# Performance work log

Hardware: AMD Instinct MI355X
Metric: run time of the kernel (lower is better)

The kernel has to match this reference:

```python
import jax, jax.numpy as jnp
import numpy as np

NEG_SLOPE = 0.01  # torch.nn.LeakyReLU default


def setup_inputs() -> dict:
    key = jax.random.key(0)
    ks = jax.random.split(key, 9)
    B, S, F1, F2, N, M, E, L = 2, 256, 512, 512, 20000, 2, 320000, 3
    x = jax.random.normal(ks[0], (B, S, F1), dtype=jnp.float32)
    nodes = jax.random.normal(ks[1], (N, M, F2), dtype=jnp.float32)
    edge_index = jax.random.randint(ks[2], (2, E), 0, N, dtype=jnp.int32)
    Wp = jax.random.normal(ks[3], (F1, F2), dtype=jnp.float32) * 0.02  # torch Linear weight [out,in]
    bp = jax.random.normal(ks[4], (F1,), dtype=jnp.float32) * 0.02
    gcn_W = jax.random.normal(ks[5], (L, S, S), dtype=jnp.float32) * 0.05  # stored as [in,out]
    gcn_b = jax.random.normal(ks[6], (L, S), dtype=jnp.float32) * 0.02
    w_bp = jax.random.normal(ks[7], (S,), dtype=jnp.float32) * 0.05
    b_bp = jax.random.normal(ks[8], (1,), dtype=jnp.float32) * 0.02
    return {"x": x, "nodes": nodes, "edge_index": edge_index, "Wp": Wp, "bp": bp,
            "gcn_W": gcn_W, "gcn_b": gcn_b, "w_bp": w_bp, "b_bp": b_bp}


def reference(x, nodes, edge_index, Wp, bp, gcn_W, gcn_b, w_bp, b_bp):
    # Eval mode: dropout layers are identity.
    N = nodes.shape[0]
    L = gcn_W.shape[0]
    proj = nodes @ Wp.T + bp                         # [N, M, F1]
    score = jnp.einsum('bsk,nmk->bsn', x, proj)      # sum over M and F1 -> [B, S, N]
    h = score.transpose(0, 2, 1)                     # beliefs [B, N, S]

    # GCN normalization with self-loops: D^{-1/2} (A + I) D^{-1/2}
    src, dst = edge_index[0], edge_index[1]
    loop = jnp.arange(N, dtype=edge_index.dtype)
    row = jnp.concatenate([src, loop])               # message sources
    col = jnp.concatenate([dst, loop])               # message targets
    deg = jnp.zeros((N,), dtype=h.dtype).at[col].add(1.0)
    dinv = deg ** -0.5                               # deg >= 1 due to self-loops
    norm = dinv[row] * dinv[col]                     # [E+N]

    for l in range(L):
        hw = h @ gcn_W[l]                            # [B, N, S]
        msg = hw[:, row, :] * norm[None, :, None]    # gather + scale
        agg = jnp.zeros_like(hw).at[:, col, :].add(msg) + gcn_b[l]
        h = jax.nn.leaky_relu(agg, NEG_SLOPE)

    # belief_projection: Linear(S, 1) then squeeze -> [B, N]
    return h @ w_bp + b_bp[0]
```

## Files before the change

kernel.cpp:

```cpp
#include <hip/hip_runtime.h>
#include <cstddef>
#include <cstdint>

#define NN 20000

typedef short frag16 __attribute__((ext_vector_type(8)));
typedef float f32x4 __attribute__((ext_vector_type(4)));

__device__ inline unsigned short f32_to_bf16(float f) {
    uint32_t u = __float_as_uint(f);
    u += 0x7FFFu + ((u >> 16) & 1u);
    return (unsigned short)(u >> 16);
}

__device__ inline void dec8_add(uint4 v, float* a) {
    a[0] += __uint_as_float(v.x << 16);
    a[1] += __uint_as_float(v.x & 0xffff0000u);
    a[2] += __uint_as_float(v.y << 16);
    a[3] += __uint_as_float(v.y & 0xffff0000u);
    a[4] += __uint_as_float(v.z << 16);
    a[5] += __uint_as_float(v.z & 0xffff0000u);
    a[6] += __uint_as_float(v.w << 16);
    a[7] += __uint_as_float(v.w & 0xffff0000u);
}

__global__ __launch_bounds__(256) void prep(
    const float* __restrict__ nodes, const float* __restrict__ x,
    const float* __restrict__ gcn_W, const float* __restrict__ bp,
    const int* __restrict__ src, const int* __restrict__ dst,
    unsigned short* __restrict__ nsum16, unsigned short* __restrict__ WT,
    float* __restrict__ Tf, float* __restrict__ cvec,
    int* __restrict__ cnt, int* __restrict__ csr, int E)
{
    __shared__ __align__(16) char shmem[8704];
    const int blk = blockIdx.x, tid = threadIdx.x;

    if (blk < 64) {
        float* As = (float*)shmem;
        float* Bs = As + 1024;
        int t = blk;
        int b = t >> 5, rem = t & 31;
        int s0 = (rem >> 3) * 64, f0 = (rem & 7) * 64;
        const float* W1 = gcn_W;
        const float* xb = x + (size_t)b * 256 * 512;
        int kk = tid >> 4, c4 = (tid & 15) << 2;
        int tm = tid >> 4, tn = tid & 15;
        float acc[4][4] = {};
        float4 av = *(const float4*)(W1 + (size_t)kk * 256 + s0 + c4);
        float4 bv = *(const float4*)(xb + (size_t)kk * 512 + f0 + c4);
        for (int k0 = 0; k0 < 256; k0 += 16) {
            __syncthreads();
            *(float4*)&As[kk * 64 + c4] = av;
            *(float4*)&Bs[kk * 64 + c4] = bv;
            __syncthreads();
            if (k0 + 16 < 256) {
                av = *(const float4*)(W1 + (size_t)(k0 + 16 + kk) * 256 + s0 + c4);
                bv = *(const float4*)(xb + (size_t)(k0 + 16 + kk) * 512 + f0 + c4);
            }
            #pragma unroll
            for (int k = 0; k < 16; ++k) {
                float a[4], bb[4];
                *(float4*)a  = *(const float4*)&As[k * 64 + (tm << 2)];
                *(float4*)bb = *(const float4*)&Bs[k * 64 + (tn << 2)];
                #pragma unroll
                for (int i = 0; i < 4; ++i)
                    #pragma unroll
                    for (int j = 0; j < 4; ++j) acc[i][j] += a[i] * bb[j];
            }
        }
        #pragma unroll
        for (int i = 0; i < 4; ++i) {
            int row = b * 256 + s0 + (tm << 2) + i;
            *(float4*)(Tf + (size_t)row * 512 + f0 + (tn << 2)) =
                make_float4(acc[i][0], acc[i][1], acc[i][2], acc[i][3]);
        }
    } else if (blk < 96) {
        unsigned short (*tsh)[68] = (unsigned short(*)[68])shmem;
        int t = blk - 64;
        int l = t >> 4, rem = t & 15;
        int c0 = (rem & 3) * 64, r0 = (rem >> 2) * 64;
        const float* inp = gcn_W + (size_t)(l + 1) * 65536;
        unsigned short* outp = WT + (size_t)l * 65536;
        int tx = tid & 15, ty = tid >> 4;
        #pragma unroll
        for (int rr = 0; rr < 4; ++rr) {
            int r = ty * 4 + rr;
            float4 v = *(const float4*)(inp + (size_t)(r0 + r) * 256 + c0 + tx * 4);
            tsh[tx * 4 + 0][r] = f32_to_bf16(v.x);
            tsh[tx * 4 + 1][r] = f32_to_bf16(v.y);
            tsh[tx * 4 + 2][r] = f32_to_bf16(v.z);
            tsh[tx * 4 + 3][r] = f32_to_bf16(v.w);
        }
        __syncthreads();
        #pragma unroll
        for (int cc = 0; cc < 4; ++cc) {
            int c = ty * 4 + cc;
            ushort4 o = *(ushort4*)&tsh[c][tx * 4];
            *(ushort4*)(outp + (size_t)(c0 + c) * 256 + r0 + tx * 4) = o;
        }
    } else if (blk < 224) {
        int row = (blk - 96) * 4 + (tid >> 6);
        int lane = tid & 63;
        const float* xr = x + (size_t)row * 512;
        float s = 0.f;
        #pragma unroll
        for (int k = 0; k < 512; k += 64) s += xr[k + lane] * bp[k + lane];
        #pragma unroll
        for (int off = 32; off; off >>= 1) s += __shfl_down(s, off);
        if (lane == 0) cvec[row] = 2.0f * s;
    } else if (blk < 224 + 2512) {
        int g = (blk - 224) * 256 + tid;
        int n = g >> 5, c = (g & 31) << 4;
        uint4 o0, o1;
        if (n < NN) {
            const float* r0 = nodes + (size_t)n * 1024 + c;
            const float* r1 = r0 + 512;
            float4 a0 = *(const float4*)(r0 + 0),  a1 = *(const float4*)(r0 + 4);
            float4 a2 = *(const float4*)(r0 + 8),  a3 = *(const float4*)(r0 + 12);
            float4 b0 = *(const float4*)(r1 + 0),  b1 = *(const float4*)(r1 + 4);
            float4 b2 = *(const float4*)(r1 + 8),  b3 = *(const float4*)(r1 + 12);
            o0.x = ((uint32_t)f32_to_bf16(a0.y + b0.y) << 16) | f32_to_bf16(a0.x + b0.x);
            o0.y = ((uint32_t)f32_to_bf16(a0.w + b0.w) << 16) | f32_to_bf16(a0.z + b0.z);
            o0.z = ((uint32_t)f32_to_bf16(a1.y + b1.y) << 16) | f32_to_bf16(a1.x + b1.x);
            o0.w = ((uint32_t)f32_to_bf16(a1.w + b1.w) << 16) | f32_to_bf16(a1.z + b1.z);
            o1.x = ((uint32_t)f32_to_bf16(a2.y + b2.y) << 16) | f32_to_bf16(a2.x + b2.x);
            o1.y = ((uint32_t)f32_to_bf16(a2.w + b2.w) << 16) | f32_to_bf16(a2.z + b2.z);
            o1.z = ((uint32_t)f32_to_bf16(a3.y + b3.y) << 16) | f32_to_bf16(a3.x + b3.x);
            o1.w = ((uint32_t)f32_to_bf16(a3.w + b3.w) << 16) | f32_to_bf16(a3.z + b3.z);
        } else {
            o0 = make_uint4(0, 0, 0, 0); o1 = o0;
        }
        *(uint4*)(nsum16 + (size_t)n * 512 + c) = o0;
        *(uint4*)(nsum16 + (size_t)n * 512 + c + 8) = o1;
    } else {
        int e = (blk - 2736) * 256 + tid;
        if (e < E) {
            int d = dst[e];
            int pos = atomicAdd(&cnt[d], 1);
            if (pos < 64) csr[(d << 6) + pos] = src[e];
        }
    }
}

__global__ __launch_bounds__(256) void mid(
    const float* __restrict__ Tf, const float* __restrict__ Wp,
    const float* __restrict__ gcn_W, const float* __restrict__ cvec,
    unsigned short* __restrict__ Ub, float* __restrict__ cb2)
{
    const int blk = blockIdx.x, tid = threadIdx.x;
    if (blk >= 64) {
        int idx = (blk - 64) * 256 + tid;
        int b = idx >> 8, s = idx & 255;
        float sum = 0.f;
        for (int sp = 0; sp < 256; ++sp)
            sum += gcn_W[(size_t)sp * 256 + s] * cvec[b * 256 + sp];
        cb2[idx] = sum;
        return;
    }
    __shared__ float As[16][68];
    __shared__ float Bs[16][64];
    int bm = (blk >> 3) * 64, bn = (blk & 7) * 64;
    int arow = tid >> 2, acol = (tid & 3) << 2;
    int brow = tid >> 4, bcol = (tid & 15) << 2;
    int tm = tid >> 4, tn = tid & 15;
    float acc[4][4] = {};
    float4 av = *(const float4*)(Tf + (size_t)(bm + arow) * 512 + acol);
    float4 bv = *(const float4*)(Wp + (size_t)brow * 512 + bn + bcol);
    for (int k0 = 0; k0 < 512; k0 += 16) {
        __syncthreads();
        As[acol + 0][arow] = av.x; As[acol + 1][arow] = av.y;
        As[acol + 2][arow] = av.z; As[acol + 3][arow] = av.w;
        *(float4*)&Bs[brow][bcol] = bv;
        __syncthreads();
        if (k0 + 16 < 512) {
            av = *(const float4*)(Tf + (size_t)(bm + arow) * 512 + k0 + 16 + acol);
            bv = *(const float4*)(Wp + (size_t)(k0 + 16 + brow) * 512 + bn + bcol);
        }
        #pragma unroll
        for (int k = 0; k < 16; ++k) {
            float a[4], b[4];
            *(float4*)a = *(const float4*)&As[k][tm << 2];
            *(float4*)b = *(const float4*)&Bs[k][tn << 2];
            #pragma unroll
            for (int i = 0; i < 4; ++i)
                #pragma unroll
                for (int j = 0; j < 4; ++j) acc[i][j] += a[i] * b[j];
        }
    }
    #pragma unroll
    for (int i = 0; i < 4; ++i) {
        int row = bm + (tm << 2) + i;
        ushort4 o;
        o.x = f32_to_bf16(acc[i][0]); o.y = f32_to_bf16(acc[i][1]);
        o.z = f32_to_bf16(acc[i][2]); o.w = f32_to_bf16(acc[i][3]);
        *(ushort4*)(Ub + (size_t)row * 512 + bn + (tn << 2)) = o;
    }
}

__global__ __launch_bounds__(256) void mgemm(
    const unsigned short* __restrict__ A, const unsigned short* __restrict__ BT,
    int K, int N, int mode,
    const float* __restrict__ cb2, const int* __restrict__ cnt,
    unsigned short* __restrict__ C)
{
    __shared__ __align__(16) unsigned short As[128 * 32];
    __shared__ __align__(16) unsigned short Bs[128 * 32];
    const int bm = blockIdx.y * 128, bn = blockIdx.x * 128;
    const int tid = threadIdx.x;
    const int lane = tid & 63, w = tid >> 6;
    const int wm = (w >> 1) << 6, wn = (w & 1) << 6;
    const int r = lane & 15, q = lane >> 4;

    f32x4 acc[4][4] = {};

    for (int k0 = 0; k0 < K; k0 += 32) {
        __syncthreads();
        #pragma unroll
        for (int t = 0; t < 2; ++t) {
            int c = t * 256 + w * 64 + lane;
            int row = c >> 2, col = (c & 3) << 3;
            __builtin_amdgcn_global_load_lds(
                (const __attribute__((address_space(1))) void*)(A + (size_t)(bm + row) * K + k0 + col),
                (__attribute__((address_space(3))) void*)(As + (size_t)(t * 256 + w * 64) * 8),
                16, 0, 0);
            __builtin_amdgcn_global_load_lds(
                (const __attribute__((address_space(1))) void*)(BT + (size_t)(bn + row) * K + k0 + col),
                (__attribute__((address_space(3))) void*)(Bs + (size_t)(t * 256 + w * 64) * 8),
                16, 0, 0);
        }
        __syncthreads();
        frag16 af[4], bf[4];
        #pragma unroll
        for (int i = 0; i < 4; ++i)
            af[i] = *(const frag16*)(As + ((wm + i * 16 + r) << 5) + (q << 3));
        #pragma unroll
        for (int j = 0; j < 4; ++j)
            bf[j] = *(const frag16*)(Bs + ((wn + j * 16 + r) << 5) + (q << 3));
        #pragma unroll
        for (int i = 0; i < 4; ++i)
            #pragma unroll
            for (int j = 0; j < 4; ++j)
                acc[i][j] = __builtin_amdgcn_mfma_f32_16x16x32_bf16(af[i], bf[j], acc[i][j], 0, 0, 0);
    }

    #pragma unroll
    for (int i = 0; i < 4; ++i) {
        #pragma unroll
        for (int rg = 0; rg < 4; ++rg) {
            int m = bm + wm + i * 16 + (q << 2) + rg;
            float sc;
            int b2 = 0, node = m;
            if (mode == 1) {
                int nc = m > NN - 1 ? NN - 1 : m;
                sc = rsqrtf((float)cnt[nc] + 1.0f);
            } else {
                b2 = m >= NN;
                node = m - b2 * NN;
                int nc = node > NN - 1 ? NN - 1 : node;
                sc = rsqrtf((float)cnt[nc] + 1.0f);
                if (node > 20095) node = 20095;
            }
            #pragma unroll
            for (int j = 0; j < 4; ++j) {
                int n = bn + wn + j * 16 + r;
                if (mode == 1) {
                    float v = (acc[i][j][rg] + cb2[n]) * sc;
                    C[(size_t)m * 512 + n] = f32_to_bf16(v);
                } else {
                    float v = acc[i][j][rg] * sc;
                    C[(size_t)node * 512 + (b2 << 8) + n] = f32_to_bf16(v);
                }
            }
        }
    }
}

__global__ __launch_bounds__(256) void aggregate_x(
    const unsigned short* __restrict__ hw, const int* __restrict__ cnt,
    const int* __restrict__ csr, const float* __restrict__ bias,
    unsigned short* __restrict__ hout,
    const float* __restrict__ w_bp, float* __restrict__ pout)
{
    __shared__ int sidx[2048];
    __shared__ int sdeg[32];
    const int s  = blockIdx.x & 7;
    const int nb = blockIdx.x >> 3;
    const int tid = threadIdx.x;
    const int g = tid >> 3;
    const int j = tid & 7;
    const int n = nb * 32 + g;

    {
        const int4* cp = (const int4*)(csr + ((size_t)nb << 11));
        int4 v0 = cp[tid * 2];
        int4 v1 = cp[tid * 2 + 1];
        *(int4*)&sidx[tid * 8]     = v0;
        *(int4*)&sidx[tid * 8 + 4] = v1;
        if (tid < 32) {
            int d = cnt[nb * 32 + tid];
            sdeg[tid] = d > 64 ? 64 : d;
        }
    }
    __syncthreads();

    const unsigned short* rowp = hw + (s << 6) + (j << 3);
    const int deg = sdeg[g];
    const int* gi = sidx + (g << 6);

    float acc[8] = {};
    dec8_add(*(const uint4*)(rowp + (size_t)n * 512), acc);

    int e = 0;
    for (; e + 8 <= deg; e += 8) {
        int s0 = gi[e + 0], s1 = gi[e + 1], s2 = gi[e + 2], s3 = gi[e + 3];
        int s4 = gi[e + 4], s5 = gi[e + 5], s6 = gi[e + 6], s7 = gi[e + 7];
        uint4 u0 = *(const uint4*)(rowp + (size_t)s0 * 512);
        uint4 u1 = *(const uint4*)(rowp + (size_t)s1 * 512);
        uint4 u2 = *(const uint4*)(rowp + (size_t)s2 * 512);
        uint4 u3 = *(const uint4*)(rowp + (size_t)s3 * 512);
        uint4 u4 = *(const uint4*)(rowp + (size_t)s4 * 512);
        uint4 u5 = *(const uint4*)(rowp + (size_t)s5 * 512);
        uint4 u6 = *(const uint4*)(rowp + (size_t)s6 * 512);
        uint4 u7 = *(const uint4*)(rowp + (size_t)s7 * 512);
        dec8_add(u0, acc); dec8_add(u1, acc); dec8_add(u2, acc); dec8_add(u3, acc);
        dec8_add(u4, acc); dec8_add(u5, acc); dec8_add(u6, acc); dec8_add(u7, acc);
    }
    for (; e < deg; ++e) {
        dec8_add(*(const uint4*)(rowp + (size_t)gi[e] * 512), acc);
    }

    float dn = rsqrtf((float)deg + 1.0f);
    int colb = ((s & 3) << 6) + (j << 3);
    float bl[8];
    *(float4*)&bl[0] = *(const float4*)(bias + colb);
    *(float4*)&bl[4] = *(const float4*)(bias + colb + 4);
    float v[8];
    #pragma unroll
    for (int t = 0; t < 8; ++t) {
        v[t] = fmaf(dn, acc[t], bl[t]);
        v[t] = v[t] > 0.f ? v[t] : 0.01f * v[t];
    }

    if (hout) {
        int b = s >> 2;
        uint4 o;
        o.x = ((uint32_t)f32_to_bf16(v[1]) << 16) | f32_to_bf16(v[0]);
        o.y = ((uint32_t)f32_to_bf16(v[3]) << 16) | f32_to_bf16(v[2]);
        o.z = ((uint32_t)f32_to_bf16(v[5]) << 16) | f32_to_bf16(v[4]);
        o.w = ((uint32_t)f32_to_bf16(v[7]) << 16) | f32_to_bf16(v[6]);
        *(uint4*)(hout + ((size_t)(b * NN + n)) * 256 + colb) = o;
    } else {
        float w4[8];
        *(float4*)&w4[0] = *(const float4*)(w_bp + colb);
        *(float4*)&w4[4] = *(const float4*)(w_bp + colb + 4);
        float sum = 0.f;
        #pragma unroll
        for (int t = 0; t < 8; ++t) sum += v[t] * w4[t];
        sum += __shfl_xor(sum, 1);
        sum += __shfl_xor(sum, 2);
        sum += __shfl_xor(sum, 4);
        if (j == 0) pout[s * NN + n] = sum;
    }
}

__global__ __launch_bounds__(256) void finishk(
    const float* __restrict__ pout, const float* __restrict__ b_bp,
    float* __restrict__ out)
{
    int i = blockIdx.x * 256 + threadIdx.x;
    if (i < 2 * NN) {
        int b = i >= NN;
        int n = i - b * NN;
        const float* p = pout + b * 4 * NN + n;
        out[i] = b_bp[0] + p[0] + p[NN] + p[2 * NN] + p[3 * NN];
    }
}

extern "C" void kernel_launch(void* const* d_in, const int* in_sizes, int n_in,
                              void* d_out, int out_size, void* d_ws, size_t ws_size,
                              hipStream_t stream) {
    const float* x     = (const float*)d_in[0];
    const float* nodes = (const float*)d_in[1];
    const int*   eidx  = (const int*)d_in[2];
    const float* Wp    = (const float*)d_in[3];
    const float* bp    = (const float*)d_in[4];
    const float* gcn_W = (const float*)d_in[5];
    const float* gcn_b = (const float*)d_in[6];
    const float* w_bp  = (const float*)d_in[7];
    const float* b_bp  = (const float*)d_in[8];
    const int E = in_sizes[2] / 2;

    char* w = (char*)d_ws;
    auto alloc = [&](size_t bytes) { char* p = w; w += (bytes + 255) & ~(size_t)255; return p; };
    unsigned short* nsum16 = (unsigned short*)alloc((size_t)20096 * 512 * 2);
    unsigned short* hw16   = (unsigned short*)alloc((size_t)20096 * 512 * 2);
    unsigned short* hA     = (unsigned short*)alloc((size_t)40192 * 256 * 2);
    unsigned short* hB     = (unsigned short*)alloc((size_t)40192 * 256 * 2);
    float* Tf  = (float*)alloc((size_t)512 * 512 * 4);
    unsigned short* Ub = (unsigned short*)alloc((size_t)512 * 512 * 2);
    unsigned short* WT = (unsigned short*)alloc((size_t)2 * 256 * 256 * 2);
    float* cvec = (float*)alloc(512 * 4);
    float* cb2  = (float*)alloc(512 * 4);
    float* pout = (float*)alloc((size_t)8 * NN * 4);
    int*   cnt  = (int*)alloc((size_t)NN * 4);
    int*   csr  = (int*)alloc((size_t)NN * 64 * 4);

    hipMemsetAsync(cnt, 0, (size_t)NN * 4, stream);

    const int cntBlks = (E + 255) / 256;
    prep<<<cntBlks + 64 + 2512 + 32 + 128, 256, 0, stream>>>(
        nodes, x, gcn_W, bp, eidx, eidx + E, nsum16, WT, Tf, cvec, cnt, csr, E);
    mid<<<66, 256, 0, stream>>>(Tf, Wp, gcn_W, cvec, Ub, cb2);

    mgemm<<<dim3(4, 157), 256, 0, stream>>>(nsum16, Ub, 512, 512, 1, cb2, cnt, hw16);

    aggregate_x<<<5000, 256, 0, stream>>>(hw16, cnt, csr, gcn_b + 0, hA, w_bp, pout);
    mgemm<<<dim3(2, 313), 256, 0, stream>>>(hA, WT, 256, 256, 2, nullptr, cnt, hw16);
    aggregate_x<<<5000, 256, 0, stream>>>(hw16, cnt, csr, gcn_b + 256, hB, w_bp, pout);
    mgemm<<<dim3(2, 313), 256, 0, stream>>>(hB, WT + 65536, 256, 256, 2, nullptr, cnt, hw16);
    aggregate_x<<<5000, 256, 0, stream>>>(hw16, cnt, csr, gcn_b + 512, nullptr, w_bp, pout);
    finishk<<<157, 256, 0, stream>>>(pout, b_bp, (float*)d_out);
}
```

Before: 339.8 us.

## Partition CSR build by destination range and deepen gather unroll in aggregation

The edge-to-CSR build moves to the front of the fused prep launch. Each edge chunk is now handled by 8 blocks, and each block only processes destinations in its own 2500-node range, so atomics and csr writes from one block stay in a narrower address region. This costs 8x redundant reads of dst. Separately, the aggregation gather loop issues 16 independent row loads per iteration instead of 8, raising memory-level parallelism at the cost of more registers.

```diff
diff --git a/kernel.cpp b/kernel.cpp
--- a/kernel.cpp
+++ b/kernel.cpp
@@ -34,11 +34,27 @@
 {
     __shared__ __align__(16) char shmem[8704];
     const int blk = blockIdx.x, tid = threadIdx.x;
-
-    if (blk < 64) {
+    const int csrB = ((E + 2047) >> 11) << 3;
+
+    if (blk < csrB) {
+        const int part = blk & 7;
+        const int ebase = (blk >> 3) << 11;
+        const int d0 = part * 2500, d1 = d0 + 2500;
+        #pragma unroll
+        for (int k = 0; k < 8; ++k) {
+            int e = ebase + k * 256 + tid;
+            if (e < E) {
+                int d = dst[e];
+                if (d >= d0 && d < d1) {
+                    int pos = atomicAdd(&cnt[d], 1);
+                    if (pos < 64) csr[(d << 6) + pos] = src[e];
+                }
+            }
+        }
+    } else if (blk < csrB + 64) {
         float* As = (float*)shmem;
         float* Bs = As + 1024;
-        int t = blk;
+        int t = blk - csrB;
         int b = t >> 5, rem = t & 31;
         int s0 = (rem >> 3) * 64, f0 = (rem & 7) * 64;
         const float* W1 = gcn_W;
@@ -74,9 +90,9 @@
             *(float4*)(Tf + (size_t)row * 512 + f0 + (tn << 2)) =
                 make_float4(acc[i][0], acc[i][1], acc[i][2], acc[i][3]);
         }
-    } else if (blk < 96) {
+    } else if (blk < csrB + 96) {
         unsigned short (*tsh)[68] = (unsigned short(*)[68])shmem;
-        int t = blk - 64;
+        int t = blk - csrB - 64;
         int l = t >> 4, rem = t & 15;
         int c0 = (rem & 3) * 64, r0 = (rem >> 2) * 64;
         const float* inp = gcn_W + (size_t)(l + 1) * 65536;
@@ -98,8 +114,8 @@
             ushort4 o = *(ushort4*)&tsh[c][tx * 4];
             *(ushort4*)(outp + (size_t)(c0 + c) * 256 + r0 + tx * 4) = o;
         }
-    } else if (blk < 224) {
-        int row = (blk - 96) * 4 + (tid >> 6);
+    } else if (blk < csrB + 224) {
+        int row = (blk - csrB - 96) * 4 + (tid >> 6);
         int lane = tid & 63;
         const float* xr = x + (size_t)row * 512;
         float s = 0.f;
@@ -108,8 +124,8 @@
         #pragma unroll
         for (int off = 32; off; off >>= 1) s += __shfl_down(s, off);
         if (lane == 0) cvec[row] = 2.0f * s;
-    } else if (blk < 224 + 2512) {
-        int g = (blk - 224) * 256 + tid;
+    } else {
+        int g = (blk - csrB - 224) * 256 + tid;
         int n = g >> 5, c = (g & 31) << 4;
         uint4 o0, o1;
         if (n < NN) {
@@ -132,13 +148,6 @@
         }
         *(uint4*)(nsum16 + (size_t)n * 512 + c) = o0;
         *(uint4*)(nsum16 + (size_t)n * 512 + c + 8) = o1;
-    } else {
-        int e = (blk - 2736) * 256 + tid;
-        if (e < E) {
-            int d = dst[e];
-            int pos = atomicAdd(&cnt[d], 1);
-            if (pos < 64) csr[(d << 6) + pos] = src[e];
-        }
     }
 }
 
@@ -311,19 +320,22 @@
     dec8_add(*(const uint4*)(rowp + (size_t)n * 512), acc);
 
     int e = 0;
-    for (; e + 8 <= deg; e += 8) {
-        int s0 = gi[e + 0], s1 = gi[e + 1], s2 = gi[e + 2], s3 = gi[e + 3];
-        int s4 = gi[e + 4], s5 = gi[e + 5], s6 = gi[e + 6], s7 = gi[e + 7];
-        uint4 u0 = *(const uint4*)(rowp + (size_t)s0 * 512);
-        uint4 u1 = *(const uint4*)(rowp + (size_t)s1 * 512);
-        uint4 u2 = *(const uint4*)(rowp + (size_t)s2 * 512);
-        uint4 u3 = *(const uint4*)(rowp + (size_t)s3 * 512);
-        uint4 u4 = *(const uint4*)(rowp + (size_t)s4 * 512);
-        uint4 u5 = *(const uint4*)(rowp + (size_t)s5 * 512);
-        uint4 u6 = *(const uint4*)(rowp + (size_t)s6 * 512);
-        uint4 u7 = *(const uint4*)(rowp + (size_t)s7 * 512);
-        dec8_add(u0, acc); dec8_add(u1, acc); dec8_add(u2, acc); dec8_add(u3, acc);
-        dec8_add(u4, acc); dec8_add(u5, acc); dec8_add(u6, acc); dec8_add(u7, acc);
+    for (; e + 16 <= deg; e += 16) {
+        uint4 u[16];
+        #pragma unroll
+        for (int t = 0; t < 16; ++t)
+            u[t] = *(const uint4*)(rowp + (size_t)gi[e + t] * 512);
+        #pragma unroll
+        for (int t = 0; t < 16; ++t) dec8_add(u[t], acc);
+    }
+    if (e + 8 <= deg) {
+        uint4 u[8];
+        #pragma unroll
+        for (int t = 0; t < 8; ++t)
+            u[t] = *(const uint4*)(rowp + (size_t)gi[e + t] * 512);
+        #pragma unroll
+        for (int t = 0; t < 8; ++t) dec8_add(u[t], acc);
+        e += 8;
     }
     for (; e < deg; ++e) {
         dec8_add(*(const uint4*)(rowp + (size_t)gi[e] * 512), acc);
@@ -407,8 +419,8 @@
 
     hipMemsetAsync(cnt, 0, (size_t)NN * 4, stream);
 
-    const int cntBlks = (E + 255) / 256;
-    prep<<<cntBlks + 64 + 2512 + 32 + 128, 256, 0, stream>>>(
+    const int csrB = ((E + 2047) / 2048) * 8;
+    prep<<<csrB + 224 + 2512, 256, 0, stream>>>(
         nodes, x, gcn_W, bp, eidx, eidx + E, nsum16, WT, Tf, cvec, cnt, csr, E);
     mid<<<66, 256, 0, stream>>>(Tf, Wp, gcn_W, cvec, Ub, cb2);
 
```

Result: slower. 359.7 us (+5.9%).

## Retile mid GEMM into smaller tiles and remap mgemm blocks per XCD

Applied to the files above, without the earlier changes.

The small fp32 GEMM in mid moves from 64 blocks with 64x64 tiles to 256 blocks with 32x32 tiles, so more CUs take part, at the cost of less register reuse and dropping the prefetch of the next k-slice. mgemm now uses a 1D grid and remaps the block id so that consecutive tiles land on the same XCD, which is meant to improve L2 locality for shared A/B rows across MI355X chiplets. The remapping also adds index arithmetic, and the tile mapping depends on the mode-specific column count.

```diff
diff --git a/kernel.cpp b/kernel.cpp
--- a/kernel.cpp
+++ b/kernel.cpp
@@ -148,8 +148,8 @@
     unsigned short* __restrict__ Ub, float* __restrict__ cb2)
 {
     const int blk = blockIdx.x, tid = threadIdx.x;
-    if (blk >= 64) {
-        int idx = (blk - 64) * 256 + tid;
+    if (blk >= 256) {
+        int idx = (blk - 256) * 256 + tid;
         int b = idx >> 8, s = idx & 255;
         float sum = 0.f;
         for (int sp = 0; sp < 256; ++sp)
@@ -157,43 +157,33 @@
         cb2[idx] = sum;
         return;
     }
-    __shared__ float As[16][68];
-    __shared__ float Bs[16][64];
-    int bm = (blk >> 3) * 64, bn = (blk & 7) * 64;
-    int arow = tid >> 2, acol = (tid & 3) << 2;
-    int brow = tid >> 4, bcol = (tid & 15) << 2;
-    int tm = tid >> 4, tn = tid & 15;
-    float acc[4][4] = {};
-    float4 av = *(const float4*)(Tf + (size_t)(bm + arow) * 512 + acol);
-    float4 bv = *(const float4*)(Wp + (size_t)brow * 512 + bn + bcol);
+    __shared__ float As[16][33];
+    __shared__ float Bs[16][34];
+    int bm = (blk >> 4) << 5, bn = (blk & 15) << 5;
+    int ar = tid >> 3, ac = (tid & 7) << 1;
+    int br = tid >> 4, bc = (tid & 15) << 1;
+    int tm = (tid >> 4) << 1, tn = (tid & 15) << 1;
+    float acc[2][2] = {};
     for (int k0 = 0; k0 < 512; k0 += 16) {
+        float2 av = *(const float2*)(Tf + (size_t)(bm + ar) * 512 + k0 + ac);
+        float2 bv = *(const float2*)(Wp + (size_t)(k0 + br) * 512 + bn + bc);
         __syncthreads();
-        As[acol + 0][arow] = av.x; As[acol + 1][arow] = av.y;
-        As[acol + 2][arow] = av.z; As[acol + 3][arow] = av.w;
-        *(float4*)&Bs[brow][bcol] = bv;
+        As[ac][ar] = av.x; As[ac + 1][ar] = av.y;
+        Bs[br][bc] = bv.x; Bs[br][bc + 1] = bv.y;
         __syncthreads();
-        if (k0 + 16 < 512) {
-            av = *(const float4*)(Tf + (size_t)(bm + arow) * 512 + k0 + 16 + acol);
-            bv = *(const float4*)(Wp + (size_t)(k0 + 16 + brow) * 512 + bn + bcol);
-        }
         #pragma unroll
         for (int k = 0; k < 16; ++k) {
-            float a[4], b[4];
-            *(float4*)a = *(const float4*)&As[k][tm << 2];
-            *(float4*)b = *(const float4*)&Bs[k][tn << 2];
-            #pragma unroll
-            for (int i = 0; i < 4; ++i)
-                #pragma unroll
-                for (int j = 0; j < 4; ++j) acc[i][j] += a[i] * b[j];
+            float a0 = As[k][tm], a1 = As[k][tm + 1];
+            float b0 = Bs[k][tn], b1 = Bs[k][tn + 1];
+            acc[0][0] += a0 * b0; acc[0][1] += a0 * b1;
+            acc[1][0] += a1 * b0; acc[1][1] += a1 * b1;
         }
     }
     #pragma unroll
-    for (int i = 0; i < 4; ++i) {
-        int row = bm + (tm << 2) + i;
-        ushort4 o;
+    for (int i = 0; i < 2; ++i) {
+        ushort2 o;
         o.x = f32_to_bf16(acc[i][0]); o.y = f32_to_bf16(acc[i][1]);
-        o.z = f32_to_bf16(acc[i][2]); o.w = f32_to_bf16(acc[i][3]);
-        *(ushort4*)(Ub + (size_t)row * 512 + bn + (tn << 2)) = o;
+        *(ushort2*)(Ub + (size_t)(bm + tm + i) * 512 + bn + tn) = o;
     }
 }
 
@@ -205,11 +195,17 @@
 {
     __shared__ __align__(16) unsigned short As[128 * 32];
     __shared__ __align__(16) unsigned short Bs[128 * 32];
-    const int bm = blockIdx.y * 128, bn = blockIdx.x * 128;
+    const int nwg = gridDim.x;
+    const int orig = blockIdx.x;
+    const int xcd = orig & 7, jj = orig >> 3;
+    const int q = nwg >> 3, r = nwg & 7;
+    const int wgid = (xcd < r ? xcd * (q + 1) : r * (q + 1) + (xcd - r) * q) + jj;
+    const int lx = (mode == 1) ? 2 : 1;
+    const int bm = (wgid >> lx) * 128, bn = (wgid & ((1 << lx) - 1)) * 128;
     const int tid = threadIdx.x;
     const int lane = tid & 63, w = tid >> 6;
     const int wm = (w >> 1) << 6, wn = (w & 1) << 6;
-    const int r = lane & 15, q = lane >> 4;
+    const int r16 = lane & 15, q16 = lane >> 4;
 
     f32x4 acc[4][4] = {};
 
@@ -232,10 +228,10 @@
         frag16 af[4], bf[4];
         #pragma unroll
         for (int i = 0; i < 4; ++i)
-            af[i] = *(const frag16*)(As + ((wm + i * 16 + r) << 5) + (q << 3));
+            af[i] = *(const frag16*)(As + ((wm + i * 16 + r16) << 5) + (q16 << 3));
         #pragma unroll
         for (int j = 0; j < 4; ++j)
-            bf[j] = *(const frag16*)(Bs + ((wn + j * 16 + r) << 5) + (q << 3));
+            bf[j] = *(const frag16*)(Bs + ((wn + j * 16 + r16) << 5) + (q16 << 3));
         #pragma unroll
         for (int i = 0; i < 4; ++i)
             #pragma unroll
@@ -247,7 +243,7 @@
     for (int i = 0; i < 4; ++i) {
         #pragma unroll
         for (int rg = 0; rg < 4; ++rg) {
-            int m = bm + wm + i * 16 + (q << 2) + rg;
+            int m = bm + wm + i * 16 + (q16 << 2) + rg;
             float sc;
             int b2 = 0, node = m;
             if (mode == 1) {
@@ -262,7 +258,7 @@
             }
             #pragma unroll
             for (int j = 0; j < 4; ++j) {
-                int n = bn + wn + j * 16 + r;
+                int n = bn + wn + j * 16 + r16;
                 if (mode == 1) {
                     float v = (acc[i][j][rg] + cb2[n]) * sc;
                     C[(size_t)m * 512 + n] = f32_to_bf16(v);
@@ -410,14 +406,14 @@
     const int cntBlks = (E + 255) / 256;
     prep<<<cntBlks + 64 + 2512 + 32 + 128, 256, 0, stream>>>(
         nodes, x, gcn_W, bp, eidx, eidx + E, nsum16, WT, Tf, cvec, cnt, csr, E);
-    mid<<<66, 256, 0, stream>>>(Tf, Wp, gcn_W, cvec, Ub, cb2);
-
-    mgemm<<<dim3(4, 157), 256, 0, stream>>>(nsum16, Ub, 512, 512, 1, cb2, cnt, hw16);
+    mid<<<258, 256, 0, stream>>>(Tf, Wp, gcn_W, cvec, Ub, cb2);
+
+    mgemm<<<628, 256, 0, stream>>>(nsum16, Ub, 512, 512, 1, cb2, cnt, hw16);
 
     aggregate_x<<<5000, 256, 0, stream>>>(hw16, cnt, csr, gcn_b + 0, hA, w_bp, pout);
-    mgemm<<<dim3(2, 313), 256, 0, stream>>>(hA, WT, 256, 256, 2, nullptr, cnt, hw16);
+    mgemm<<<626, 256, 0, stream>>>(hA, WT, 256, 256, 2, nullptr, cnt, hw16);
     aggregate_x<<<5000, 256, 0, stream>>>(hw16, cnt, csr, gcn_b + 256, hB, w_bp, pout);
-    mgemm<<<dim3(2, 313), 256, 0, stream>>>(hB, WT + 65536, 256, 256, 2, nullptr, cnt, hw16);
+    mgemm<<<626, 256, 0, stream>>>(hB, WT + 65536, 256, 256, 2, nullptr, cnt, hw16);
     aggregate_x<<<5000, 256, 0, stream>>>(hw16, cnt, csr, gcn_b + 512, nullptr, w_bp, pout);
     finishk<<<157, 256, 0, stream>>>(pout, b_bp, (float*)d_out);
 }
```

New measurement: 345.6 us. No clear change (+1.7%).

## Load MFMA fragments directly from global memory and shrink mgemm N-tile

Applied to the files above, without the earlier changes.

Removes the LDS staging and both barriers per k-step from the bf16 MFMA GEMM. Each wave now reads its A and B fragments straight from global memory into registers. The block tile drops from 128x128 to 128x64, and the grid doubles in x to compensate. The goal is to cut synchronization and LDS traffic and to raise the block count, at the cost of relying on L1/L2 for cross-wave reuse and issuing more global loads.

```diff
diff --git a/kernel.cpp b/kernel.cpp
--- a/kernel.cpp
+++ b/kernel.cpp
@@ -203,43 +203,31 @@
     const float* __restrict__ cb2, const int* __restrict__ cnt,
     unsigned short* __restrict__ C)
 {
-    __shared__ __align__(16) unsigned short As[128 * 32];
-    __shared__ __align__(16) unsigned short Bs[128 * 32];
-    const int bm = blockIdx.y * 128, bn = blockIdx.x * 128;
+    const int bm = blockIdx.y * 128, bn = blockIdx.x * 64;
     const int tid = threadIdx.x;
     const int lane = tid & 63, w = tid >> 6;
-    const int wm = (w >> 1) << 6, wn = (w & 1) << 6;
-    const int r = lane & 15, q = lane >> 4;
-
-    f32x4 acc[4][4] = {};
-
+    const int wm = (w >> 1) << 6, wn = (w & 1) << 5;
+    const int r16 = lane & 15, q16 = lane >> 4;
+
+    const unsigned short* Ap = A  + (size_t)(bm + wm + r16) * K + (q16 << 3);
+    const unsigned short* Bp = BT + (size_t)(bn + wn + r16) * K + (q16 << 3);
+    const size_t a16 = (size_t)16 * K;
+
+    f32x4 acc[4][2] = {};
+
+    #pragma unroll 2
     for (int k0 = 0; k0 < K; k0 += 32) {
-        __syncthreads();
-        #pragma unroll
-        for (int t = 0; t < 2; ++t) {
-            int c = t * 256 + w * 64 + lane;
-            int row = c >> 2, col = (c & 3) << 3;
-            __builtin_amdgcn_global_load_lds(
-                (const __attribute__((address_space(1))) void*)(A + (size_t)(bm + row) * K + k0 + col),
-                (__attribute__((address_space(3))) void*)(As + (size_t)(t * 256 + w * 64) * 8),
-                16, 0, 0);
-            __builtin_amdgcn_global_load_lds(
-                (const __attribute__((address_space(1))) void*)(BT + (size_t)(bn + row) * K + k0 + col),
-                (__attribute__((address_space(3))) void*)(Bs + (size_t)(t * 256 + w * 64) * 8),
-                16, 0, 0);
-        }
-        __syncthreads();
-        frag16 af[4], bf[4];
-        #pragma unroll
-        for (int i = 0; i < 4; ++i)
-            af[i] = *(const frag16*)(As + ((wm + i * 16 + r) << 5) + (q << 3));
-        #pragma unroll
-        for (int j = 0; j < 4; ++j)
-            bf[j] = *(const frag16*)(Bs + ((wn + j * 16 + r) << 5) + (q << 3));
+        frag16 af[4], bf[2];
+        af[0] = *(const frag16*)(Ap + k0);
+        af[1] = *(const frag16*)(Ap + a16 + k0);
+        af[2] = *(const frag16*)(Ap + 2 * a16 + k0);
+        af[3] = *(const frag16*)(Ap + 3 * a16 + k0);
+        bf[0] = *(const frag16*)(Bp + k0);
+        bf[1] = *(const frag16*)(Bp + a16 + k0);
         #pragma unroll
         for (int i = 0; i < 4; ++i)
             #pragma unroll
-            for (int j = 0; j < 4; ++j)
+            for (int j = 0; j < 2; ++j)
                 acc[i][j] = __builtin_amdgcn_mfma_f32_16x16x32_bf16(af[i], bf[j], acc[i][j], 0, 0, 0);
     }
 
@@ -247,7 +235,7 @@
     for (int i = 0; i < 4; ++i) {
         #pragma unroll
         for (int rg = 0; rg < 4; ++rg) {
-            int m = bm + wm + i * 16 + (q << 2) + rg;
+            int m = bm + wm + i * 16 + (q16 << 2) + rg;
             float sc;
             int b2 = 0, node = m;
             if (mode == 1) {
@@ -261,8 +249,8 @@
                 if (node > 20095) node = 20095;
             }
             #pragma unroll
-            for (int j = 0; j < 4; ++j) {
-                int n = bn + wn + j * 16 + r;
+            for (int j = 0; j < 2; ++j) {
+                int n = bn + wn + j * 16 + r16;
                 if (mode == 1) {
                     float v = (acc[i][j][rg] + cb2[n]) * sc;
                     C[(size_t)m * 512 + n] = f32_to_bf16(v);
@@ -412,12 +400,12 @@
         nodes, x, gcn_W, bp, eidx, eidx + E, nsum16, WT, Tf, cvec, cnt, csr, E);
     mid<<<66, 256, 0, stream>>>(Tf, Wp, gcn_W, cvec, Ub, cb2);
 
-    mgemm<<<dim3(4, 157), 256, 0, stream>>>(nsum16, Ub, 512, 512, 1, cb2, cnt, hw16);
+    mgemm<<<dim3(8, 157), 256, 0, stream>>>(nsum16, Ub, 512, 512, 1, cb2, cnt, hw16);
 
     aggregate_x<<<5000, 256, 0, stream>>>(hw16, cnt, csr, gcn_b + 0, hA, w_bp, pout);
-    mgemm<<<dim3(2, 313), 256, 0, stream>>>(hA, WT, 256, 256, 2, nullptr, cnt, hw16);
+    mgemm<<<dim3(4, 314), 256, 0, stream>>>(hA, WT, 256, 256, 2, nullptr, cnt, hw16);
     aggregate_x<<<5000, 256, 0, stream>>>(hw16, cnt, csr, gcn_b + 256, hB, w_bp, pout);
-    mgemm<<<dim3(2, 313), 256, 0, stream>>>(hB, WT + 65536, 256, 256, 2, nullptr, cnt, hw16);
+    mgemm<<<dim3(4, 314), 256, 0, stream>>>(hB, WT + 65536, 256, 256, 2, nullptr, cnt, hw16);
     aggregate_x<<<5000, 256, 0, stream>>>(hw16, cnt, csr, gcn_b + 512, nullptr, w_bp, pout);
     finishk<<<157, 256, 0, stream>>>(pout, b_bp, (float*)d_out);
 }
```

Result: slower. 405.1 us (+19.2%).
